# Performance work log

Measured on AMD Instinct MI355X. Metric: run time of the kernel, lower is better.

Reference implementation:

```python
import jax, jax.numpy as jnp
import numpy as np

B, N, D = 8, 1024, 1024

def setup_inputs() -> dict:
    key = jax.random.key(0)
    k1, k2, k3, k4, k5 = jax.random.split(key, 5)
    x = jax.random.normal(k1, (B, N, D), dtype=jnp.float32)
    y = jax.random.normal(k2, (B, N, D), dtype=jnp.float32)
    adj = jax.random.uniform(k3, (B, N, N), dtype=jnp.float32)
    adj_sumrow = jnp.sum(adj, axis=-1, keepdims=True)  # [B, N, 1], row-sum normalizer
    W = jax.random.normal(k4, (D, D), dtype=jnp.float32) * (1.0 / np.sqrt(D))
    b = jax.random.normal(k5, (D,), dtype=jnp.float32) * 0.02
    return {"x": x, "y": y, "adj": adj, "adj_sumrow": adj_sumrow, "W": W, "b": b}

def reference(x, y, adj, adj_sumrow, W, b):
    # GraphConvolutionCustom: project neighbor features, aggregate via dense adj,
    # normalize by row-sum, add bias and residual input x; then ReLU.
    # Dropout is identity in eval mode (training=False).
    support = jnp.einsum('bnd,de->bne', y, W)          # [B, N, D]
    agg = jnp.matmul(adj, support) / adj_sumrow        # [B, N, D]
    out = jax.nn.relu(agg + b + x)
    return out
```

## Files before the change

kernel.cpp:

```cpp
#include <hip/hip_runtime.h>
#include <hip/hip_bf16.h>
#include <stdint.h>


typedef float  f32x4  __attribute__((ext_vector_type(4)));
typedef __bf16 bf16x8 __attribute__((ext_vector_type(8)));

__device__ __forceinline__ unsigned short f2bf(float f) {
  union { float f; unsigned int u; } c; c.f = f;
  unsigned int u = c.u;
  u += 0x7FFFu + ((u >> 16) & 1u);
  return (unsigned short)(u >> 16);
}

__device__ __forceinline__ void async_cp16(const void* g, void* l) {
  __builtin_amdgcn_global_load_lds(
      (const __attribute__((address_space(1))) unsigned int*)g,
      (__attribute__((address_space(3))) unsigned int*)l, 16, 0, 0);
}


__global__ void k_cvt(const float4* __restrict__ src, ushort4* __restrict__ dst, int n4) {
  int i = blockIdx.x * blockDim.x + threadIdx.x;
  if (i >= n4) return;
  float4 v = src[i];
  ushort4 p;
  p.x = f2bf(v.x); p.y = f2bf(v.y); p.z = f2bf(v.z); p.w = f2bf(v.w);
  dst[i] = p;
}

__global__ void k_transpose_cvt(const float* __restrict__ W, unsigned short* __restrict__ Wt) {
  __shared__ float t[64][65];
  const int tx = threadIdx.x, ty = threadIdx.y;
  const int n0 = blockIdx.x * 64, k0 = blockIdx.y * 64;
#pragma unroll
  for (int r = ty; r < 64; r += 4)
    t[r][tx] = W[(size_t)(k0 + r) * 1024 + n0 + tx];
  __syncthreads();
#pragma unroll
  for (int r = ty; r < 64; r += 4)
    Wt[(size_t)(n0 + r) * 1024 + k0 + tx] = f2bf(t[tx][r]);
}


__device__ __forceinline__ void gemm_mainloop64(
    const unsigned short* __restrict__ A,  int strideA,
    const unsigned short* __restrict__ Bt, int strideB,
    int m0, int n0, f32x4 acc[4][4],
    unsigned short* lA, unsigned short* lB, int tid)
{
  const int lane = tid & 63;
  const int wave = tid >> 6;
  const int wm   = (wave >> 1) * 64;
  const int wn   = (wave & 1) * 64;
  const int quad = lane >> 4;
  const int l16  = lane & 15;
  const int rg   = lane >> 3;
  const int colo = (((lane & 7) - rg) & 7) * 8;

#pragma unroll 1
  for (int k0 = 0; k0 < 1024; k0 += 64) {
#pragma unroll
    for (int s = 0; s < 4; ++s) {
      const int t = wave * 4 + s;
      async_cp16(A  + (size_t)(m0 + t * 8 + rg) * strideA + k0 + colo, lA + t * 512);
      async_cp16(Bt + (size_t)(n0 + t * 8 + rg) * strideB + k0 + colo, lB + t * 512);
    }
    __syncthreads();

#pragma unroll
    for (int h = 0; h < 2; ++h) {
      bf16x8 af[4], bfr[4];
#pragma unroll
      for (int i = 0; i < 4; ++i) {
        const int r = wm + i * 16 + l16;
        af[i]  = *(const bf16x8*)(lA + r * 64 + ((h * 4 + quad + r) & 7) * 8);
      }
#pragma unroll
      for (int j = 0; j < 4; ++j) {
        const int r = wn + j * 16 + l16;
        bfr[j] = *(const bf16x8*)(lB + r * 64 + ((h * 4 + quad + r) & 7) * 8);
      }
#pragma unroll
      for (int i = 0; i < 4; ++i)
#pragma unroll
        for (int j = 0; j < 4; ++j)
          acc[i][j] = __builtin_amdgcn_mfma_f32_16x16x32_bf16(af[i], bfr[j], acc[i][j], 0, 0, 0);
    }
    __syncthreads();
  }
}

__device__ __forceinline__ void zero_acc(f32x4 acc[4][4]) {
#pragma unroll
  for (int i = 0; i < 4; ++i)
#pragma unroll
    for (int j = 0; j < 4; ++j)
#pragma unroll
      for (int r = 0; r < 4; ++r) acc[i][j][r] = 0.0f;
}


__global__ __launch_bounds__(256) void k_gemm1(
    const unsigned short* __restrict__ Wt,
    const unsigned short* __restrict__ Ybf,
    unsigned short* __restrict__ Sup2)
{
  __shared__ __align__(16) unsigned short lA[128 * 64];
  __shared__ __align__(16) unsigned short lB[128 * 64];
  const int tid = threadIdx.x;
  const int n0 = blockIdx.x * 128, m0 = blockIdx.y * 128;

  f32x4 acc[4][4];
  zero_acc(acc);
  gemm_mainloop64(Wt, 1024, Ybf, 1024, m0, n0, acc, lA, lB, tid);

  const int lane = tid & 63, wave = tid >> 6;
  const int wm = (wave >> 1) * 64, wn = (wave & 1) * 64;
  const int quad = lane >> 4, l16 = lane & 15;
#pragma unroll
  for (int i = 0; i < 4; ++i) {
    const int mb = m0 + wm + i * 16 + quad * 4;
#pragma unroll
    for (int r = 0; r < 4; ++r) {
      unsigned short* row = Sup2 + ((size_t)(mb + r) << 13);
#pragma unroll
      for (int j = 0; j < 4; ++j)
        row[n0 + wn + j * 16 + l16] = f2bf(acc[i][j][r]);
    }
  }
}


__global__ __launch_bounds__(256) void k_gemm2(
    const unsigned short* __restrict__ AdjBf,
    const unsigned short* __restrict__ Sup2,
    const float* __restrict__ x,
    const float* __restrict__ sumrow,
    const float* __restrict__ bias,
    float* __restrict__ out)
{
  __shared__ __align__(16) unsigned short lA[128 * 64];
  __shared__ __align__(16) unsigned short lB[128 * 64];
  const int tid = threadIdx.x;
  const int n0 = blockIdx.x * 128, m0 = blockIdx.y * 128, b = blockIdx.z;

  f32x4 acc[4][4];
  zero_acc(acc);
  gemm_mainloop64(AdjBf + ((size_t)b << 20), 1024,
                  Sup2 + ((size_t)b << 10), 8192,
                  m0, n0, acc, lA, lB, tid);

  const float* xb = x   + ((size_t)b << 20);
  float*       ob = out + ((size_t)b << 20);
  const float* sr = sumrow + ((size_t)b << 10);
  const int lane = tid & 63, wave = tid >> 6;
  const int wm = (wave >> 1) * 64, wn = (wave & 1) * 64;
  const int quad = lane >> 4, l16 = lane & 15;

  float bv[4];
#pragma unroll
  for (int j = 0; j < 4; ++j) bv[j] = bias[n0 + wn + j * 16 + l16];

#pragma unroll
  for (int i = 0; i < 4; ++i) {
    const int mb = m0 + wm + i * 16 + quad * 4;
#pragma unroll
    for (int r = 0; r < 4; ++r) {
      const int m = mb + r;
      const float inv = 1.0f / sr[m];
#pragma unroll
      for (int j = 0; j < 4; ++j) {
        const int n = n0 + wn + j * 16 + l16;
        const size_t idx = (((size_t)m) << 10) + n;
        float v = acc[i][j][r] * inv + bv[j] + xb[idx];
        ob[idx] = fmaxf(v, 0.0f);
      }
    }
  }
}


extern "C" void kernel_launch(void* const* d_in, const int* in_sizes, int n_in,
                              void* d_out, int out_size, void* d_ws, size_t ws_size,
                              hipStream_t stream) {
  const float* x      = (const float*)d_in[0];
  const float* y      = (const float*)d_in[1];
  const float* adj    = (const float*)d_in[2];
  const float* sumrow = (const float*)d_in[3];
  const float* W      = (const float*)d_in[4];
  const float* bias   = (const float*)d_in[5];
  float* out = (float*)d_out;

  char* ws = (char*)d_ws;
  unsigned short* ybf   = (unsigned short*)(ws);
  unsigned short* adjbf = (unsigned short*)(ws + ((size_t)16 << 20));
  unsigned short* wt    = (unsigned short*)(ws + ((size_t)32 << 20));
  unsigned short* sup2  = (unsigned short*)(ws + ((size_t)34 << 20));

  const int n4 = (8 << 20) / 4;
  k_cvt<<<dim3(n4 / 256), dim3(256), 0, stream>>>((const float4*)y,   (ushort4*)ybf,   n4);
  k_cvt<<<dim3(n4 / 256), dim3(256), 0, stream>>>((const float4*)adj, (ushort4*)adjbf, n4);
  k_transpose_cvt<<<dim3(16, 16), dim3(64, 4), 0, stream>>>(W, wt);
  k_gemm1<<<dim3(64, 8), dim3(256), 0, stream>>>(wt, ybf, sup2);
  k_gemm2<<<dim3(8, 8, 8), dim3(256), 0, stream>>>(adjbf, sup2, x, sumrow, bias, out);
}
```

Measured before the change: 207.1 us.

## Double-buffer LDS in GEMM mainloop and merge prep kernels into one launch

Both GEMMs now use two LDS buffers: the next 64-wide K tile is loaded asynchronously while the current tile is multiplied. Manual vmcnt waits and raw s_barrier replace the load-then-compute __syncthreads pattern. Separately, the two fp32-to-bf16 conversions and the W transpose are fused into one kernel launch to save launch overhead. LDS per block doubles to 64 KB, which may lower occupancy, and the hand-written waitcnt counts rely on the assumed order of issued loads.

After: 197.0 us. 1.05x faster.

```diff
diff --git a/kernel.cpp b/kernel.cpp
--- a/kernel.cpp
+++ b/kernel.cpp
@@ -19,75 +19,110 @@
       (__attribute__((address_space(3))) unsigned int*)l, 16, 0, 0);
 }
 
-
-__global__ void k_cvt(const float4* __restrict__ src, ushort4* __restrict__ dst, int n4) {
-  int i = blockIdx.x * blockDim.x + threadIdx.x;
-  if (i >= n4) return;
-  float4 v = src[i];
-  ushort4 p;
-  p.x = f2bf(v.x); p.y = f2bf(v.y); p.z = f2bf(v.z); p.w = f2bf(v.w);
-  dst[i] = p;
-}
-
-__global__ void k_transpose_cvt(const float* __restrict__ W, unsigned short* __restrict__ Wt) {
+__device__ __forceinline__ void bar() { asm volatile("s_barrier" ::: "memory"); }
+
+
+__global__ __launch_bounds__(256) void k_prep(
+    const float4* __restrict__ y4, const float4* __restrict__ a4,
+    ushort4* __restrict__ yb, ushort4* __restrict__ ab,
+    const float* __restrict__ W, unsigned short* __restrict__ Wt)
+{
   __shared__ float t[64][65];
-  const int tx = threadIdx.x, ty = threadIdx.y;
-  const int n0 = blockIdx.x * 64, k0 = blockIdx.y * 64;
-#pragma unroll
-  for (int r = ty; r < 64; r += 4)
-    t[r][tx] = W[(size_t)(k0 + r) * 1024 + n0 + tx];
-  __syncthreads();
-#pragma unroll
-  for (int r = ty; r < 64; r += 4)
-    Wt[(size_t)(n0 + r) * 1024 + k0 + tx] = f2bf(t[tx][r]);
-}
-
-
-__device__ __forceinline__ void gemm_mainloop64(
-    const unsigned short* __restrict__ A,  int strideA,
-    const unsigned short* __restrict__ Bt, int strideB,
-    int m0, int n0, f32x4 acc[4][4],
-    unsigned short* lA, unsigned short* lB, int tid)
-{
-  const int lane = tid & 63;
-  const int wave = tid >> 6;
-  const int wm   = (wave >> 1) * 64;
-  const int wn   = (wave & 1) * 64;
-  const int quad = lane >> 4;
-  const int l16  = lane & 15;
-  const int rg   = lane >> 3;
+  const int bid = blockIdx.x;
+  if (bid < 16384) {
+    const int i = bid * 256 + threadIdx.x;
+    const bool isY = i < 2097152;
+    const float4 v = isY ? y4[i] : a4[i - 2097152];
+    ushort4 p;
+    p.x = f2bf(v.x); p.y = f2bf(v.y); p.z = f2bf(v.z); p.w = f2bf(v.w);
+    if (isY) yb[i] = p; else ab[i - 2097152] = p;
+  } else {
+    const int id = bid - 16384;
+    const int n0 = (id & 15) * 64, k0 = (id >> 4) * 64;
+    const int tx = threadIdx.x & 63, ty = threadIdx.x >> 6;
+#pragma unroll
+    for (int r = ty; r < 64; r += 4)
+      t[r][tx] = W[(size_t)(k0 + r) * 1024 + n0 + tx];
+    __syncthreads();
+#pragma unroll
+    for (int r = ty; r < 64; r += 4)
+      Wt[(size_t)(n0 + r) * 1024 + k0 + tx] = f2bf(t[tx][r]);
+  }
+}
+
+
+__device__ __forceinline__ void stage64(
+    const unsigned short* __restrict__ A,  int sA,
+    const unsigned short* __restrict__ Bt, int sB,
+    int m0, int n0, int k0,
+    unsigned short* la, unsigned short* lb,
+    int wave, int rg, int colo)
+{
+#pragma unroll
+  for (int s = 0; s < 4; ++s) {
+    const int t = wave * 4 + s;
+    async_cp16(A  + (size_t)(m0 + t * 8 + rg) * sA + k0 + colo, la + t * 512);
+    async_cp16(Bt + (size_t)(n0 + t * 8 + rg) * sB + k0 + colo, lb + t * 512);
+  }
+}
+
+__device__ __forceinline__ void compute64(
+    const unsigned short* la, const unsigned short* lb,
+    f32x4 acc[4][4], int wm, int wn, int quad, int l16)
+{
+#pragma unroll
+  for (int h = 0; h < 2; ++h) {
+    bf16x8 af[4], bfr[4];
+#pragma unroll
+    for (int i = 0; i < 4; ++i) {
+      const int r = wm + i * 16 + l16;
+      af[i] = *(const bf16x8*)(la + r * 64 + ((h * 4 + quad + r) & 7) * 8);
+    }
+#pragma unroll
+    for (int j = 0; j < 4; ++j) {
+      const int r = wn + j * 16 + l16;
+      bfr[j] = *(const bf16x8*)(lb + r * 64 + ((h * 4 + quad + r) & 7) * 8);
+    }
+#pragma unroll
+    for (int i = 0; i < 4; ++i)
+#pragma unroll
+      for (int j = 0; j < 4; ++j)
+        acc[i][j] = __builtin_amdgcn_mfma_f32_16x16x32_bf16(af[i], bfr[j], acc[i][j], 0, 0, 0);
+  }
+}
+
+__device__ __forceinline__ void gemm_dbuf(
+    const unsigned short* __restrict__ A,  int sA,
+    const unsigned short* __restrict__ Bt, int sB,
+    int m0, int n0, f32x4 acc[4][4], unsigned short* lsm, int tid)
+{
+  const int lane = tid & 63, wave = tid >> 6;
+  const int wm = (wave >> 1) * 64, wn = (wave & 1) * 64;
+  const int quad = lane >> 4, l16 = lane & 15;
+  const int rg = lane >> 3;
   const int colo = (((lane & 7) - rg) & 7) * 8;
-
+  unsigned short* la0 = lsm;
+  unsigned short* lb0 = lsm + 8192;
+  unsigned short* la1 = lsm + 16384;
+  unsigned short* lb1 = lsm + 24576;
+
+  stage64(A, sA, Bt, sB, m0, n0, 0, la0, lb0, wave, rg, colo);
 #pragma unroll 1
-  for (int k0 = 0; k0 < 1024; k0 += 64) {
-#pragma unroll
-    for (int s = 0; s < 4; ++s) {
-      const int t = wave * 4 + s;
-      async_cp16(A  + (size_t)(m0 + t * 8 + rg) * strideA + k0 + colo, lA + t * 512);
-      async_cp16(Bt + (size_t)(n0 + t * 8 + rg) * strideB + k0 + colo, lB + t * 512);
-    }
-    __syncthreads();
-
-#pragma unroll
-    for (int h = 0; h < 2; ++h) {
-      bf16x8 af[4], bfr[4];
-#pragma unroll
-      for (int i = 0; i < 4; ++i) {
-        const int r = wm + i * 16 + l16;
-        af[i]  = *(const bf16x8*)(lA + r * 64 + ((h * 4 + quad + r) & 7) * 8);
-      }
-#pragma unroll
-      for (int j = 0; j < 4; ++j) {
-        const int r = wn + j * 16 + l16;
-        bfr[j] = *(const bf16x8*)(lB + r * 64 + ((h * 4 + quad + r) & 7) * 8);
-      }
-#pragma unroll
-      for (int i = 0; i < 4; ++i)
-#pragma unroll
-        for (int j = 0; j < 4; ++j)
-          acc[i][j] = __builtin_amdgcn_mfma_f32_16x16x32_bf16(af[i], bfr[j], acc[i][j], 0, 0, 0);
-    }
-    __syncthreads();
+  for (int k0 = 0; k0 < 1024; k0 += 128) {
+    stage64(A, sA, Bt, sB, m0, n0, k0 + 64, la1, lb1, wave, rg, colo);
+    asm volatile("s_waitcnt vmcnt(8)" ::: "memory");
+    bar();
+    compute64(la0, lb0, acc, wm, wn, quad, l16);
+    bar();
+    if (k0 + 128 < 1024) {
+      stage64(A, sA, Bt, sB, m0, n0, k0 + 128, la0, lb0, wave, rg, colo);
+      asm volatile("s_waitcnt vmcnt(8)" ::: "memory");
+    } else {
+      asm volatile("s_waitcnt vmcnt(0)" ::: "memory");
+    }
+    bar();
+    compute64(la1, lb1, acc, wm, wn, quad, l16);
+    bar();
   }
 }
 
@@ -106,14 +141,13 @@
     const unsigned short* __restrict__ Ybf,
     unsigned short* __restrict__ Sup2)
 {
-  __shared__ __align__(16) unsigned short lA[128 * 64];
-  __shared__ __align__(16) unsigned short lB[128 * 64];
+  __shared__ __align__(16) unsigned short lsm[4 * 8192];
   const int tid = threadIdx.x;
   const int n0 = blockIdx.x * 128, m0 = blockIdx.y * 128;
 
   f32x4 acc[4][4];
   zero_acc(acc);
-  gemm_mainloop64(Wt, 1024, Ybf, 1024, m0, n0, acc, lA, lB, tid);
+  gemm_dbuf(Wt, 1024, Ybf, 1024, m0, n0, acc, lsm, tid);
 
   const int lane = tid & 63, wave = tid >> 6;
   const int wm = (wave >> 1) * 64, wn = (wave & 1) * 64;
@@ -140,16 +174,15 @@
     const float* __restrict__ bias,
     float* __restrict__ out)
 {
-  __shared__ __align__(16) unsigned short lA[128 * 64];
-  __shared__ __align__(16) unsigned short lB[128 * 64];
+  __shared__ __align__(16) unsigned short lsm[4 * 8192];
   const int tid = threadIdx.x;
   const int n0 = blockIdx.x * 128, m0 = blockIdx.y * 128, b = blockIdx.z;
 
   f32x4 acc[4][4];
   zero_acc(acc);
-  gemm_mainloop64(AdjBf + ((size_t)b << 20), 1024,
-                  Sup2 + ((size_t)b << 10), 8192,
-                  m0, n0, acc, lA, lB, tid);
+  gemm_dbuf(AdjBf + ((size_t)b << 20), 1024,
+            Sup2 + ((size_t)b << 10), 8192,
+            m0, n0, acc, lsm, tid);
 
   const float* xb = x   + ((size_t)b << 20);
   float*       ob = out + ((size_t)b << 20);
@@ -198,10 +231,8 @@
   unsigned short* wt    = (unsigned short*)(ws + ((size_t)32 << 20));
   unsigned short* sup2  = (unsigned short*)(ws + ((size_t)34 << 20));
 
-  const int n4 = (8 << 20) / 4;
-  k_cvt<<<dim3(n4 / 256), dim3(256), 0, stream>>>((const float4*)y,   (ushort4*)ybf,   n4);
-  k_cvt<<<dim3(n4 / 256), dim3(256), 0, stream>>>((const float4*)adj, (ushort4*)adjbf, n4);
-  k_transpose_cvt<<<dim3(16, 16), dim3(64, 4), 0, stream>>>(W, wt);
+  k_prep<<<dim3(16640), dim3(256), 0, stream>>>(
+      (const float4*)y, (const float4*)adj, (ushort4*)ybf, (ushort4*)adjbf, W, wt);
   k_gemm1<<<dim3(64, 8), dim3(256), 0, stream>>>(wt, ybf, sup2);
   k_gemm2<<<dim3(8, 8, 8), dim3(256), 0, stream>>>(adjbf, sup2, x, sumrow, bias, out);
 }
```
